# Performance work log

Hardware: AMD Instinct MI355X
Metric: run time of the kernel (lower is better)

Reference implementation:

```python
import jax, jax.numpy as jnp
import numpy as np

MAXGRAD = 2.0


def _forward(im, defgrad, affine):
    B, H, W, C = im.shape
    dt = im.dtype
    c = jnp.asarray(MAXGRAD, dt)
    # logistic growth: c / (1 + (c-1) * exp(-x)), maps defgrad into (0, c)
    dg = c / (1.0 + (c - 1.0) * jnp.exp(-defgrad))
    # integral image -> monotone sampling grid
    x_s = jnp.cumsum(dg[..., 0], axis=2)  # cumulate along width
    y_s = jnp.cumsum(dg[..., 1], axis=1)  # cumulate along height
    grid = jnp.stack([x_s, y_s], axis=-1)  # [B,H,W,2]
    # residual affine: affine + identity, applied in homogeneous coords
    ident = jnp.array([1, 0, 0, 0, 1, 0, 0, 0, 1], dtype=dt)
    A = (affine.reshape(-1, 9) + ident).reshape(B, 3, 3)
    grid3 = jnp.concatenate([grid, jnp.ones((B, H, W, 1), dt)], axis=-1)
    grid3 = jnp.einsum('bhwk,bjk->bhwj', grid3, A)  # matmul(grid, A^T)
    x = grid3[..., 0]
    y = grid3[..., 1]
    # bilinear sampling with clamped corner indices
    x0 = jnp.clip(jnp.floor(x).astype(jnp.int32), 0, W - 1)
    x1 = jnp.clip(jnp.floor(x).astype(jnp.int32) + 1, 0, W - 1)
    y0 = jnp.clip(jnp.floor(y).astype(jnp.int32), 0, H - 1)
    y1 = jnp.clip(jnp.floor(y).astype(jnp.int32) + 1, 0, H - 1)
    bidx = jnp.arange(B, dtype=jnp.int32)[:, None, None]  # batch base index
    Ia = im[bidx, y0, x0]  # [B,H,W,C]
    Ib = im[bidx, y1, x0]
    Ic = im[bidx, y0, x1]
    Id = im[bidx, y1, x1]
    x0f = x0.astype(dt); x1f = x1.astype(dt)
    y0f = y0.astype(dt); y1f = y1.astype(dt)
    wa = ((x1f - x) * (y1f - y))[..., None]
    wb = ((x1f - x) * (y - y0f))[..., None]
    wc = ((x - x0f) * (y1f - y))[..., None]
    wd = ((x - x0f) * (y - y0f))[..., None]
    out = wa * Ia + wb * Ib + wc * Ic + wd * Id
    return out, grid3


def setup_inputs() -> dict:
    key = jax.random.key(0)
    k1, k2, k3 = jax.random.split(key, 3)
    B, H, W, C = 16, 512, 512, 4
    im = jax.random.normal(k1, (B, H, W, C), dtype=jnp.float32)
    defgrad = jax.random.normal(k2, (B, H, W, 2), dtype=jnp.float32)
    affine = jax.random.normal(k3, (B, 9), dtype=jnp.float32) * 0.01
    return {"im": im, "defgrad": defgrad, "affine": affine}


def reference(im, defgrad, affine):
    return _forward(im, defgrad, affine)
```

## Files before the change

### kernel.cpp

```cpp
#include <hip/hip_runtime.h>
#include <math.h>

#define BB 16
#define HH 512
#define WW 512
#define CC 4

__global__ __launch_bounds__(512)
void colscan_kernel(const float2* __restrict__ defgrad, float* __restrict__ ys,
                    int ys_stride) {
    const int wt  = blockIdx.x % (WW / 32);
    const int b   = blockIdx.x / (WW / 32);
    const int col = threadIdx.x & 31;
    const int seg = threadIdx.x >> 5;
    const int SEGH = HH / 16;
    const int w  = wt * 32 + col;
    const int h0 = seg * SEGH;
    const float2* dg = defgrad + (size_t)b * HH * WW;

    float vals[SEGH];
    float s = 0.f;
#pragma unroll
    for (int i = 0; i < SEGH; ++i) {
        float v = dg[(size_t)(h0 + i) * WW + w].y;
        v = 2.0f / (1.0f + expf(-v));
        vals[i] = v;
        s += v;
    }

    __shared__ float part[16][32];
    part[seg][col] = s;
    __syncthreads();

    float run = 0.f;
    for (int j = 0; j < seg; ++j) run += part[j][col];

    const size_t rowbase = ((size_t)b * HH + h0) * WW + w;
#pragma unroll
    for (int i = 0; i < SEGH; ++i) {
        run += vals[i];
        ys[(rowbase + (size_t)i * WW) * (size_t)ys_stride] = run;
    }
}

__global__ __launch_bounds__(512)
void rowscan_sample_kernel(const float4* __restrict__ im4,
                           const float2* __restrict__ defgrad,
                           const float*  __restrict__ affine,
                           const float*  __restrict__ ys, int ys_stride,
                           float4* __restrict__ out4,
                           float*  __restrict__ grid3) {
    const int h = blockIdx.x % HH;
    const int b = blockIdx.x / HH;
    const int w = threadIdx.x;
    const size_t pix = ((size_t)b * HH + h) * WW + w;

    float vx  = defgrad[pix].x;
    float dgx = 2.0f / (1.0f + expf(-vx));

    const int lane = w & 63;
    const int wv   = w >> 6;
    float x = dgx;
#pragma unroll
    for (int off = 1; off < 64; off <<= 1) {
        float n = __shfl_up(x, off, 64);
        if (lane >= off) x += n;
    }
    __shared__ float wsum[8];
    if (lane == 63) wsum[wv] = x;
    __syncthreads();
    float pref = 0.f;
    for (int j = 0; j < wv; ++j) pref += wsum[j];
    const float xs = x + pref;

    const float ysv = ys[pix * (size_t)ys_stride];

    const float* Ab = affine + b * 9;
    const float xg = (Ab[0] + 1.f) * xs + Ab[1] * ysv + Ab[2];
    const float yg = Ab[3] * xs + (Ab[4] + 1.f) * ysv + Ab[5];
    const float wg = Ab[6] * xs + Ab[7] * ysv + (Ab[8] + 1.f);

    const int ix = (int)floorf(xg);
    const int iy = (int)floorf(yg);
    const int x0 = min(max(ix,     0), WW - 1);
    const int x1 = min(max(ix + 1, 0), WW - 1);
    const int y0 = min(max(iy,     0), HH - 1);
    const int y1 = min(max(iy + 1, 0), HH - 1);
    const float x0f = (float)x0, x1f = (float)x1;
    const float y0f = (float)y0, y1f = (float)y1;
    const float wa = (x1f - xg) * (y1f - yg);
    const float wb = (x1f - xg) * (yg - y0f);
    const float wc = (xg - x0f) * (y1f - yg);
    const float wd = (xg - x0f) * (yg - y0f);

    const size_t base = (size_t)b * HH * WW;
    const float4 Ia = im4[base + (size_t)y0 * WW + x0];
    const float4 Ib = im4[base + (size_t)y1 * WW + x0];
    const float4 Ic = im4[base + (size_t)y0 * WW + x1];
    const float4 Id = im4[base + (size_t)y1 * WW + x1];

    float4 o;
    o.x = wa * Ia.x + wb * Ib.x + wc * Ic.x + wd * Id.x;
    o.y = wa * Ia.y + wb * Ib.y + wc * Ic.y + wd * Id.y;
    o.z = wa * Ia.z + wb * Ib.z + wc * Ic.z + wd * Id.z;
    o.w = wa * Ia.w + wb * Ib.w + wc * Ic.w + wd * Id.w;
    out4[pix] = o;

    grid3[pix * 3 + 0] = xg;
    grid3[pix * 3 + 1] = yg;
    grid3[pix * 3 + 2] = wg;
}

extern "C" void kernel_launch(void* const* d_in, const int* in_sizes, int n_in,
                              void* d_out, int out_size, void* d_ws, size_t ws_size,
                              hipStream_t stream) {
    const float* im      = (const float*)d_in[0];
    const float* defgrad = (const float*)d_in[1];
    const float* affine  = (const float*)d_in[2];

    float* out   = (float*)d_out;
    float* grid3 = out + (size_t)BB * HH * WW * CC;

    const size_t ys_bytes = (size_t)BB * HH * WW * sizeof(float);
    float* ys;
    int ys_stride;
    if (ws_size >= ys_bytes) {
        ys = (float*)d_ws;
        ys_stride = 1;
    } else {
        ys = grid3 + 1;
        ys_stride = 3;
    }

    colscan_kernel<<<BB * (WW / 32), 512, 0, stream>>>(
        (const float2*)defgrad, ys, ys_stride);

    rowscan_sample_kernel<<<BB * HH, 512, 0, stream>>>(
        (const float4*)im, (const float2*)defgrad, affine,
        ys, ys_stride, (float4*)out, grid3);
}
```

Before: 258.1 us.

## Precompute x logistic in column-scan kernel and process multiple rows per sample block

The column-scan kernel now reads the full float2 defgrad and also writes the logistic-transformed x component to a workspace plane. This lets the sampling kernel drop its second defgrad read and exp. The scan kernel is widened to 1024 threads with 32 segments. The sampling kernel now handles 4 rows per block, swizzles block order across 8 groups, and hoists the affine loads. The cost is an extra intermediate write and read of the dgx plane (or strided grid3 reuse), plus an extra barrier per row.

```diff
diff --git a/kernel.cpp b/kernel.cpp
--- a/kernel.cpp
+++ b/kernel.cpp
@@ -6,38 +6,44 @@
 #define WW 512
 #define CC 4
 
-__global__ __launch_bounds__(512)
-void colscan_kernel(const float2* __restrict__ defgrad, float* __restrict__ ys,
-                    int ys_stride) {
+#define SEGS 32
+#define RPT  (HH / SEGS)
+#define RROWS 4
+
+__global__ __launch_bounds__(1024)
+void prep_colscan_kernel(const float2* __restrict__ defgrad,
+                         float* __restrict__ dgx, int dgx_stride,
+                         float* __restrict__ ys,  int ys_stride) {
     const int wt  = blockIdx.x % (WW / 32);
     const int b   = blockIdx.x / (WW / 32);
     const int col = threadIdx.x & 31;
     const int seg = threadIdx.x >> 5;
-    const int SEGH = HH / 16;
-    const int w  = wt * 32 + col;
-    const int h0 = seg * SEGH;
+    const int w   = wt * 32 + col;
+    const int h0  = seg * RPT;
     const float2* dg = defgrad + (size_t)b * HH * WW;
+    const size_t rowbase = ((size_t)b * HH + h0) * WW + w;
 
-    float vals[SEGH];
+    float vals[RPT];
     float s = 0.f;
 #pragma unroll
-    for (int i = 0; i < SEGH; ++i) {
-        float v = dg[(size_t)(h0 + i) * WW + w].y;
-        v = 2.0f / (1.0f + expf(-v));
-        vals[i] = v;
-        s += v;
+    for (int i = 0; i < RPT; ++i) {
+        float2 v = dg[(size_t)(h0 + i) * WW + w];
+        float gx = 2.0f / (1.0f + expf(-v.x));
+        float gy = 2.0f / (1.0f + expf(-v.y));
+        dgx[(rowbase + (size_t)i * WW) * (size_t)dgx_stride] = gx;
+        vals[i] = gy;
+        s += gy;
     }
 
-    __shared__ float part[16][32];
+    __shared__ float part[SEGS][32];
     part[seg][col] = s;
     __syncthreads();
 
     float run = 0.f;
     for (int j = 0; j < seg; ++j) run += part[j][col];
 
-    const size_t rowbase = ((size_t)b * HH + h0) * WW + w;
 #pragma unroll
-    for (int i = 0; i < SEGH; ++i) {
+    for (int i = 0; i < RPT; ++i) {
         run += vals[i];
         ys[(rowbase + (size_t)i * WW) * (size_t)ys_stride] = run;
     }
@@ -45,70 +51,82 @@
 
 __global__ __launch_bounds__(512)
 void rowscan_sample_kernel(const float4* __restrict__ im4,
-                           const float2* __restrict__ defgrad,
+                           const float*  __restrict__ dgx, int dgx_stride,
+                           const float*  __restrict__ ys,  int ys_stride,
                            const float*  __restrict__ affine,
-                           const float*  __restrict__ ys, int ys_stride,
                            float4* __restrict__ out4,
                            float*  __restrict__ grid3) {
-    const int h = blockIdx.x % HH;
-    const int b = blockIdx.x / HH;
-    const int w = threadIdx.x;
-    const size_t pix = ((size_t)b * HH + h) * WW + w;
+    const int blk  = blockIdx.x;
+    const int gt   = (blk & 7) * ((BB * HH / RROWS) / 8) + (blk >> 3);
+    const int tile = gt % (HH / RROWS);
+    const int b    = gt / (HH / RROWS);
 
-    float vx  = defgrad[pix].x;
-    float dgx = 2.0f / (1.0f + expf(-vx));
-
+    const int w    = threadIdx.x;
     const int lane = w & 63;
     const int wv   = w >> 6;
-    float x = dgx;
-#pragma unroll
-    for (int off = 1; off < 64; off <<= 1) {
-        float n = __shfl_up(x, off, 64);
-        if (lane >= off) x += n;
-    }
+
     __shared__ float wsum[8];
-    if (lane == 63) wsum[wv] = x;
-    __syncthreads();
-    float pref = 0.f;
-    for (int j = 0; j < wv; ++j) pref += wsum[j];
-    const float xs = x + pref;
-
-    const float ysv = ys[pix * (size_t)ys_stride];
 
     const float* Ab = affine + b * 9;
-    const float xg = (Ab[0] + 1.f) * xs + Ab[1] * ysv + Ab[2];
-    const float yg = Ab[3] * xs + (Ab[4] + 1.f) * ysv + Ab[5];
-    const float wg = Ab[6] * xs + Ab[7] * ysv + (Ab[8] + 1.f);
+    const float a00 = Ab[0] + 1.f, a01 = Ab[1], a02 = Ab[2];
+    const float a10 = Ab[3], a11 = Ab[4] + 1.f, a12 = Ab[5];
+    const float a20 = Ab[6], a21 = Ab[7], a22 = Ab[8] + 1.f;
 
-    const int ix = (int)floorf(xg);
-    const int iy = (int)floorf(yg);
-    const int x0 = min(max(ix,     0), WW - 1);
-    const int x1 = min(max(ix + 1, 0), WW - 1);
-    const int y0 = min(max(iy,     0), HH - 1);
-    const int y1 = min(max(iy + 1, 0), HH - 1);
-    const float x0f = (float)x0, x1f = (float)x1;
-    const float y0f = (float)y0, y1f = (float)y1;
-    const float wa = (x1f - xg) * (y1f - yg);
-    const float wb = (x1f - xg) * (yg - y0f);
-    const float wc = (xg - x0f) * (y1f - yg);
-    const float wd = (xg - x0f) * (yg - y0f);
+    const size_t ibase = (size_t)b * HH * WW;
 
-    const size_t base = (size_t)b * HH * WW;
-    const float4 Ia = im4[base + (size_t)y0 * WW + x0];
-    const float4 Ib = im4[base + (size_t)y1 * WW + x0];
-    const float4 Ic = im4[base + (size_t)y0 * WW + x1];
-    const float4 Id = im4[base + (size_t)y1 * WW + x1];
+    for (int r = 0; r < RROWS; ++r) {
+        const int h = tile * RROWS + r;
+        const size_t pix = ibase + (size_t)h * WW + w;
 
-    float4 o;
-    o.x = wa * Ia.x + wb * Ib.x + wc * Ic.x + wd * Id.x;
-    o.y = wa * Ia.y + wb * Ib.y + wc * Ic.y + wd * Id.y;
-    o.z = wa * Ia.z + wb * Ib.z + wc * Ic.z + wd * Id.z;
-    o.w = wa * Ia.w + wb * Ib.w + wc * Ic.w + wd * Id.w;
-    out4[pix] = o;
+        float x = dgx[pix * (size_t)dgx_stride];
+#pragma unroll
+        for (int off = 1; off < 64; off <<= 1) {
+            float n = __shfl_up(x, off, 64);
+            if (lane >= off) x += n;
+        }
+        if (lane == 63) wsum[wv] = x;
+        __syncthreads();
+        float pref = 0.f;
+        for (int j = 0; j < wv; ++j) pref += wsum[j];
+        const float xs = x + pref;
 
-    grid3[pix * 3 + 0] = xg;
-    grid3[pix * 3 + 1] = yg;
-    grid3[pix * 3 + 2] = wg;
+        const float ysv = ys[pix * (size_t)ys_stride];
+
+        const float xg = a00 * xs + a01 * ysv + a02;
+        const float yg = a10 * xs + a11 * ysv + a12;
+        const float wg = a20 * xs + a21 * ysv + a22;
+
+        const int ix = (int)floorf(xg);
+        const int iy = (int)floorf(yg);
+        const int x0 = min(max(ix,     0), WW - 1);
+        const int x1 = min(max(ix + 1, 0), WW - 1);
+        const int y0 = min(max(iy,     0), HH - 1);
+        const int y1 = min(max(iy + 1, 0), HH - 1);
+        const float x0f = (float)x0, x1f = (float)x1;
+        const float y0f = (float)y0, y1f = (float)y1;
+        const float wa = (x1f - xg) * (y1f - yg);
+        const float wb = (x1f - xg) * (yg - y0f);
+        const float wc = (xg - x0f) * (y1f - yg);
+        const float wd = (xg - x0f) * (yg - y0f);
+
+        const float4 Ia = im4[ibase + (size_t)y0 * WW + x0];
+        const float4 Ib = im4[ibase + (size_t)y1 * WW + x0];
+        const float4 Ic = im4[ibase + (size_t)y0 * WW + x1];
+        const float4 Id = im4[ibase + (size_t)y1 * WW + x1];
+
+        float4 o;
+        o.x = wa * Ia.x + wb * Ib.x + wc * Ic.x + wd * Id.x;
+        o.y = wa * Ia.y + wb * Ib.y + wc * Ic.y + wd * Id.y;
+        o.z = wa * Ia.z + wb * Ib.z + wc * Ic.z + wd * Id.z;
+        o.w = wa * Ia.w + wb * Ib.w + wc * Ic.w + wd * Id.w;
+        out4[pix] = o;
+
+        grid3[pix * 3 + 0] = xg;
+        grid3[pix * 3 + 1] = yg;
+        grid3[pix * 3 + 2] = wg;
+
+        __syncthreads();
+    }
 }
 
 extern "C" void kernel_launch(void* const* d_in, const int* in_sizes, int n_in,
@@ -121,21 +139,26 @@
     float* out   = (float*)d_out;
     float* grid3 = out + (size_t)BB * HH * WW * CC;
 
-    const size_t ys_bytes = (size_t)BB * HH * WW * sizeof(float);
-    float* ys;
-    int ys_stride;
-    if (ws_size >= ys_bytes) {
-        ys = (float*)d_ws;
-        ys_stride = 1;
+    const size_t plane = (size_t)BB * HH * WW;
+    const size_t plane_bytes = plane * sizeof(float);
+
+    float* ys;  int ys_stride;
+    float* dgx; int dgx_stride;
+    if (ws_size >= 2 * plane_bytes) {
+        ys  = (float*)d_ws;            ys_stride  = 1;
+        dgx = (float*)d_ws + plane;    dgx_stride = 1;
+    } else if (ws_size >= plane_bytes) {
+        ys  = (float*)d_ws;            ys_stride  = 1;
+        dgx = grid3 + 0;               dgx_stride = 3;
     } else {
-        ys = grid3 + 1;
-        ys_stride = 3;
+        ys  = grid3 + 1;               ys_stride  = 3;
+        dgx = grid3 + 0;               dgx_stride = 3;
     }
 
-    colscan_kernel<<<BB * (WW / 32), 512, 0, stream>>>(
-        (const float2*)defgrad, ys, ys_stride);
+    prep_colscan_kernel<<<BB * (WW / 32), 1024, 0, stream>>>(
+        (const float2*)defgrad, dgx, dgx_stride, ys, ys_stride);
 
-    rowscan_sample_kernel<<<BB * HH, 512, 0, stream>>>(
-        (const float4*)im, (const float2*)defgrad, affine,
-        ys, ys_stride, (float4*)out, grid3);
+    rowscan_sample_kernel<<<BB * (HH / RROWS), 512, 0, stream>>>(
+        (const float4*)im, dgx, dgx_stride, ys, ys_stride, affine,
+        (float4*)out, grid3);
 }
```

Measured after the change: 261.3 us. No clear change (+1.2%).
